# Kernel tuning notes

Measured on AMD Instinct MI355X. Metric: run time of the kernel, lower is better.

Reference implementation:

```python
import jax, jax.numpy as jnp
import numpy as np

HID = 257

def _lstm_cell(x, h, c, wih, whh, bih, bhh):
    # PyTorch gate order: i, f, g, o
    g = wih @ x + bih + whh @ h + bhh
    i, f, gg, o = jnp.split(g, 4)
    c2 = jax.nn.sigmoid(f) * c + jax.nn.sigmoid(i) * jnp.tanh(gg)
    h2 = jax.nn.sigmoid(o) * jnp.tanh(c2)
    return h2, c2

def _bilstm(x, state, p):
    # seq_len==1 bidirectional LSTM: fwd and bwd cells both see the single step
    hf, cf, hb, cb = state
    hf2, cf2 = _lstm_cell(x, hf, cf, p[0], p[1], p[2], p[3])
    hb2, cb2 = _lstm_cell(x, hb, cb, p[4], p[5], p[6], p[7])
    return jnp.concatenate([hf2, hb2]), (hf2, cf2, hb2, cb2)

def _conv_relu(x, w, b):
    y = jax.lax.conv_general_dilated(x, w, (1, 1), 'VALID', dimension_numbers=('NCHW', 'OIHW', 'NCHW'))
    return jax.nn.relu(y + b[None, :, None, None])

def _forward(src, conv1_w, conv1_b, conv2_w, conv2_b, conv3_w, conv3_b, conv4_w, conv4_b,
             conv5_w, conv5_b, conv6_w, conv6_b, fc1_w, fc1_b, fc2_w, fc2_b, fc3_w, fc3_b,
             enc_wih_f, enc_whh_f, enc_bih_f, enc_bhh_f, enc_wih_b, enc_whh_b, enc_bih_b, enc_bhh_b,
             dec_wih_f, dec_whh_f, dec_bih_f, dec_bhh_f, dec_wih_b, dec_whh_b, dec_bih_b, dec_bhh_b,
             lin_w, lin_b, maxlinelen):
    # AdaptiveMaxPool2d(32) on 128x128 == 4x4/stride-4 max pool
    x = src.reshape(1, 32, 32, 4, 32, 4).max(axis=(3, 5))
    x = _conv_relu(x, conv1_w, conv1_b)   # (1,64,30,30)
    x = _conv_relu(x, conv2_w, conv2_b)   # (1,128,28,28)
    x = _conv_relu(x, conv3_w, conv3_b)   # (1,256,26,26)
    x = _conv_relu(x, conv4_w, conv4_b)   # (1,512,24,24)
    x = _conv_relu(x, conv5_w, conv5_b)   # (1,512,22,22)
    x = _conv_relu(x, conv6_w, conv6_b)   # (1,512,21,21) (k=2)
    # AdaptiveMaxPool2d(10) on 21x21 == window-3/stride-2 max pool
    x = jax.lax.reduce_window(x, -jnp.inf, jax.lax.max, (1, 1, 3, 3), (1, 1, 2, 2), 'VALID')
    x = x.reshape(-1)                     # (51200,)
    x = jax.nn.relu(fc1_w @ x + fc1_b)
    x = jax.nn.relu(fc2_w @ x + fc2_b)
    feat = fc3_w @ x + fc3_b              # (128,)
    enc_p = (enc_wih_f, enc_whh_f, enc_bih_f, enc_bhh_f, enc_wih_b, enc_whh_b, enc_bih_b, enc_bhh_b)
    dec_p = (dec_wih_f, dec_whh_f, dec_bih_f, dec_bhh_f, dec_wih_b, dec_whh_b, dec_bih_b, dec_bhh_b)
    z = jnp.zeros((HID,), src.dtype)
    y, enc_state = _bilstm(feat, (z, z, z, z), enc_p)  # encode, zero init state
    x = lin_w @ y + lin_b
    y, state = _bilstm(x, enc_state, dec_p)            # decode seeded with encode hidden
    x = lin_w @ y + lin_b                              # out[0]
    def step(carry, _):
        xc, st = carry
        yy, st2 = _bilstm(xc, st, dec_p)
        x2 = lin_w @ yy + lin_b
        return (x2, st2), x2
    _, rest = jax.lax.scan(step, (x, state), None, length=maxlinelen - 1)
    return jnp.concatenate([x[None, :], rest], axis=0)  # (maxlinelen, 257)

def setup_inputs():
    key = jax.random.key(0)
    ks = iter(jax.random.split(key, 64))
    def W(shape, fan):
        return jax.random.normal(next(ks), shape, jnp.float32) / np.float32(np.sqrt(fan))
    d = {}
    d['src'] = jax.random.normal(next(ks), (1, 32, 128, 128), jnp.float32)
    convs = [(64, 32, 3), (128, 64, 3), (256, 128, 3), (512, 256, 3), (512, 512, 3), (512, 512, 2)]
    for i, (o, c, k) in enumerate(convs, 1):
        d['conv%d_w' % i] = W((o, c, k, k), c * k * k)
        d['conv%d_b' % i] = jnp.zeros((o,), jnp.float32)
    d['fc1_w'] = W((2048, 51200), 51200); d['fc1_b'] = jnp.zeros((2048,), jnp.float32)
    d['fc2_w'] = W((512, 2048), 2048);    d['fc2_b'] = jnp.zeros((512,), jnp.float32)
    d['fc3_w'] = W((128, 512), 512);      d['fc3_b'] = jnp.zeros((128,), jnp.float32)
    for pre, nin in (('enc', 128), ('dec', HID)):
        for dr in ('f', 'b'):
            d['%s_wih_%s' % (pre, dr)] = W((4 * HID, nin), HID)
            d['%s_whh_%s' % (pre, dr)] = W((4 * HID, HID), HID)
            d['%s_bih_%s' % (pre, dr)] = jnp.zeros((4 * HID,), jnp.float32)
            d['%s_bhh_%s' % (pre, dr)] = jnp.zeros((4 * HID,), jnp.float32)
    d['lin_w'] = W((HID, 2 * HID), 2 * HID)
    d['lin_b'] = jnp.zeros((HID,), jnp.float32)
    d['maxlinelen'] = 128
    return d

def reference(src, conv1_w, conv1_b, conv2_w, conv2_b, conv3_w, conv3_b, conv4_w, conv4_b,
              conv5_w, conv5_b, conv6_w, conv6_b, fc1_w, fc1_b, fc2_w, fc2_b, fc3_w, fc3_b,
              enc_wih_f, enc_whh_f, enc_bih_f, enc_bhh_f, enc_wih_b, enc_whh_b, enc_bih_b, enc_bhh_b,
              dec_wih_f, dec_whh_f, dec_bih_f, dec_bhh_f, dec_wih_b, dec_whh_b, dec_bih_b, dec_bhh_b,
              lin_w, lin_b, maxlinelen):
    return _forward(src, conv1_w, conv1_b, conv2_w, conv2_b, conv3_w, conv3_b, conv4_w, conv4_b,
                    conv5_w, conv5_b, conv6_w, conv6_b, fc1_w, fc1_b, fc2_w, fc2_b, fc3_w, fc3_b,
                    enc_wih_f, enc_whh_f, enc_bih_f, enc_bhh_f, enc_wih_b, enc_whh_b, enc_bih_b, enc_bhh_b,
                    dec_wih_f, dec_whh_f, dec_bih_f, dec_bhh_f, dec_wih_b, dec_whh_b, dec_bih_b, dec_bhh_b,
                    lin_w, lin_b, maxlinelen)
```

## Files before the change

kernel.cpp:

```cpp
#include <hip/hip_runtime.h>

#define DIV_UP(a,b) (((a)+(b)-1)/(b))
#define DEC_NWG 33

__device__ __forceinline__ float sigm(float x){ return 1.f/(1.f+__expf(-x)); }
__device__ __forceinline__ float tanh_f(float x){ return 1.f - 2.f/(__expf(2.f*x)+1.f); }

__device__ __forceinline__ void fma4x4(const float4 wv, const float4 xv, float acc[4][4]){
  acc[0][0] += wv.x*xv.x; acc[0][1] += wv.x*xv.y; acc[0][2] += wv.x*xv.z; acc[0][3] += wv.x*xv.w;
  acc[1][0] += wv.y*xv.x; acc[1][1] += wv.y*xv.y; acc[1][2] += wv.y*xv.z; acc[1][3] += wv.y*xv.w;
  acc[2][0] += wv.z*xv.x; acc[2][1] += wv.z*xv.y; acc[2][2] += wv.z*xv.z; acc[2][3] += wv.z*xv.w;
  acc[3][0] += wv.w*xv.x; acc[3][1] += wv.w*xv.y; acc[3][2] += wv.w*xv.z; acc[3][3] += wv.w*xv.w;
}

__global__ void k_setup(float* zreg, int n, int* cnt){
  int idx = threadIdx.x;
  if (idx == 0) *cnt = 0;
  for (int i = idx; i < n; i += 256) zreg[i] = 0.f;
}

__global__ void k_pool1(const float* __restrict__ src, float* __restrict__ out){
  int idx = blockIdx.x*256 + threadIdx.x;
  if (idx >= 32*32*32) return;
  int x = idx & 31, y = (idx>>5)&31, c = idx>>10;
  const float* p = src + ((size_t)(c*128) + y*4)*128 + x*4;
  float m = -1e30f;
  #pragma unroll
  for (int i=0;i<4;i++)
    #pragma unroll
    for (int j=0;j<4;j++) m = fmaxf(m, p[i*128+j]);
  out[idx] = m;
}

template<int KS>
__global__ __launch_bounds__(256) void k_conv_gemm(
    const float* __restrict__ in, const float* __restrict__ w,
    float* __restrict__ part,
    int Cin, int Hin, int Win, int Cout, int Hout, int Wout, int G, int kchunk)
{
  const int P = Hout*Wout;
  const int K = Cin*KS*KS;
  const int pxT = (P+63)>>6;
  int b = blockIdx.x;
  const int g = b % G; b /= G;
  const int pt = b % pxT; const int ot = b / pxT;
  const int k0 = g*kchunk;
  const int k1 = min(K, k0+kchunk);
  const int tid = threadIdx.x;
  const int tx = tid & 15, ty = tid >> 4;
  const int sp = tid & 63, sk = tid >> 6;
  int p_st = pt*64 + sp;
  bool pv = p_st < P;
  int pys = 0, pxs = 0;
  if (pv){ pys = p_st / Wout; pxs = p_st - pys*Wout; }
  __shared__ __align__(16) float Xs[16][64];
  __shared__ __align__(16) float Ws[16][68];
  float acc[4][4];
  #pragma unroll
  for (int i=0;i<4;i++)
    #pragma unroll
    for (int j=0;j<4;j++) acc[i][j]=0.f;
  for (int kb=k0; kb<k1; kb+=16){
    #pragma unroll
    for (int i=0;i<4;i++){
      int k = kb + sk + i*4;
      float v = 0.f;
      if (k < k1 && pv){
        int ic = k/(KS*KS); int t = k - ic*(KS*KS); int ky = t/KS, kx = t - ky*KS;
        v = in[((size_t)(ic*Hin) + pys+ky)*Win + (pxs+kx)];
      }
      Xs[sk+i*4][sp] = v;
    }
    #pragma unroll
    for (int i=0;i<4;i++){
      int k = kb + tx;
      int oc = ot*64 + ty + i*16;
      Ws[tx][ty+i*16] = (k < k1) ? w[(size_t)oc*K + k] : 0.f;
    }
    __syncthreads();
    #pragma unroll
    for (int kk=0;kk<16;kk++){
      float4 wv = *(const float4*)&Ws[kk][ty*4];
      float4 xv = *(const float4*)&Xs[kk][tx*4];
      fma4x4(wv, xv, acc);
    }
    __syncthreads();
  }
  float* po = part + (size_t)g*Cout*P;
  #pragma unroll
  for (int i=0;i<4;i++){
    int oc = ot*64 + ty*4 + i;
    #pragma unroll
    for (int j=0;j<4;j++){
      int p = pt*64 + tx*4 + j;
      if (p < P) po[(size_t)oc*P + p] = acc[i][j];
    }
  }
}

__global__ void k_conv_reduce(const float* __restrict__ part, const float* __restrict__ bias,
                              float* __restrict__ out, int Cout, int P, int G){
  int idx = blockIdx.x*256 + threadIdx.x;
  int total = Cout*P;
  if (idx >= total) return;
  int oc = idx / P;
  float s = bias[oc];
  for (int g=0; g<G; g++) s += part[(size_t)g*total + idx];
  out[idx] = fmaxf(s, 0.f);
}

__global__ void k_pool2(const float* __restrict__ in, float* __restrict__ out){
  int idx = blockIdx.x*256 + threadIdx.x;
  if (idx >= 51200) return;
  int x = idx % 10; int y = (idx/10)%10; int c = idx/100;
  const float* p = in + ((size_t)(c*21) + y*2)*21 + x*2;
  float m = -1e30f;
  #pragma unroll
  for (int i=0;i<3;i++)
    #pragma unroll
    for (int j=0;j<3;j++) m = fmaxf(m, p[i*21+j]);
  out[idx] = m;
}

__global__ __launch_bounds__(256) void k_fc(const float* __restrict__ w, const float* __restrict__ x,
                     const float* __restrict__ b, float* __restrict__ out, int N, int do_relu){
  int row = blockIdx.x;
  int tid = threadIdx.x;
  const float* wr = w + (size_t)row*N;
  float s = 0.f;
  for (int i = tid*4; i < N; i += 1024){
    float4 wv = *(const float4*)(wr + i);
    float4 xv = *(const float4*)(x + i);
    s += wv.x*xv.x + wv.y*xv.y + wv.z*xv.z + wv.w*xv.w;
  }
  #pragma unroll
  for (int off=32; off; off>>=1) s += __shfl_xor(s, off, 64);
  __shared__ float red[4];
  if ((tid & 63) == 0) red[tid>>6] = s;
  __syncthreads();
  if (tid == 0){
    float t = red[0]+red[1]+red[2]+red[3] + b[row];
    if (do_relu) t = fmaxf(t, 0.f);
    out[row] = t;
  }
}

__global__ __launch_bounds__(256) void k_gemm_wl(
    const float* __restrict__ wf, const float* __restrict__ wb,
    const float* __restrict__ lw, float* __restrict__ C)
{
  int b = blockIdx.x;
  int nt = b % 9; int mt = b / 9;
  int tid = threadIdx.x;
  int tx = tid&15, ty = tid>>4;
  int sp = tid&63, sk = tid>>6;
  __shared__ __align__(16) float Xs[16][64];
  __shared__ __align__(16) float Ws[16][68];
  float acc[4][4];
  #pragma unroll
  for (int i=0;i<4;i++)
    #pragma unroll
    for (int j=0;j<4;j++) acc[i][j]=0.f;
  for (int kb=0; kb<257; kb+=16){
    #pragma unroll
    for (int i=0;i<4;i++){
      int k = kb+sk+i*4;
      int col = nt*64 + sp;
      Xs[sk+i*4][sp] = (k<257 && col<514) ? lw[(size_t)k*514+col] : 0.f;
    }
    #pragma unroll
    for (int i=0;i<4;i++){
      int k = kb+tx;
      int row = mt*64 + ty + i*16;
      float v = 0.f;
      if (k<257 && row<2056)
        v = (row<1028) ? wf[(size_t)row*257+k] : wb[(size_t)(row-1028)*257+k];
      Ws[tx][ty+i*16] = v;
    }
    __syncthreads();
    #pragma unroll
    for (int kk=0;kk<16;kk++){
      float4 wv = *(const float4*)&Ws[kk][ty*4];
      float4 xv = *(const float4*)&Xs[kk][tx*4];
      fma4x4(wv, xv, acc);
    }
    __syncthreads();
  }
  #pragma unroll
  for (int i=0;i<4;i++){
    int row = mt*64 + ty*4 + i;
    #pragma unroll
    for (int j=0;j<4;j++){
      int col = nt*64 + tx*4 + j;
      if (row<2056 && col<514) C[(size_t)row*514+col] = acc[i][j];
    }
  }
}

__global__ void k_assemble(const float* __restrict__ C, const float* __restrict__ whf,
                           const float* __restrict__ whb, float* __restrict__ A){
  int idx = blockIdx.x*256+threadIdx.x;
  if (idx >= 528*4*576) return;
  int k = idx % 576;
  int g = (idx/576)&3;
  int u = idx/2304;
  float v = 0.f;
  if (u < 514 && k < 514){
    int j = (u<257)? u : u-257;
    int row = ((u<257)?0:1028) + g*257 + j;
    v = C[(size_t)row*514 + k];
    if (u<257){ if (k<257) v += whf[(size_t)(g*257+j)*257 + k]; }
    else      { if (k>=257) v += whb[(size_t)(g*257+j)*257 + (k-257)]; }
  }
  A[idx] = v;
}

__global__ void k_dvec(const float* __restrict__ wihf, const float* __restrict__ wihb,
                       const float* __restrict__ bihf, const float* __restrict__ bhhf,
                       const float* __restrict__ bihb, const float* __restrict__ bhhb,
                       const float* __restrict__ lb, float* __restrict__ dv){
  int idx = blockIdx.x*256+threadIdx.x;
  if (idx >= 528*4) return;
  int u = idx>>2, g = idx&3;
  float v = 0.f;
  if (u < 514){
    int j = (u<257)? u : u-257;
    int r = g*257+j;
    const float* wr = ((u<257)? wihf : wihb) + (size_t)r*257;
    v = (u<257) ? (bihf[r]+bhhf[r]) : (bihb[r]+bhhb[r]);
    for (int m=0;m<257;m++) v += wr[m]*lb[m];
  }
  dv[idx]=v;
}

__global__ void k_enc_gates(const float* __restrict__ wf, const float* __restrict__ wb,
                            const float* __restrict__ bihf, const float* __restrict__ bhhf,
                            const float* __restrict__ bihb, const float* __restrict__ bhhb,
                            const float* __restrict__ feat, float* __restrict__ gates){
  __shared__ float fs[128];
  int tid = threadIdx.x;
  if (tid < 128) fs[tid] = feat[tid];
  __syncthreads();
  int r = blockIdx.x*256 + tid;
  if (r >= 2056) return;
  const float* wr; float bias;
  if (r < 1028){ wr = wf + (size_t)r*128; bias = bihf[r]+bhhf[r]; }
  else { int rr = r-1028; wr = wb + (size_t)rr*128; bias = bihb[rr]+bhhb[rr]; }
  float s = bias;
  for (int m=0;m<128;m++) s += wr[m]*fs[m];
  gates[r] = s;
}

__global__ void k_enc_point(const float* __restrict__ gates, float* __restrict__ y0,
                            float* __restrict__ cinit){
  int u = blockIdx.x*256+threadIdx.x;
  if (u >= 514) return;
  int j = (u<257)? u : u-257;
  int base = (u<257)? 0 : 1028;
  float gi = gates[base + j];
  float gg = gates[base + 514 + j];
  float go = gates[base + 771 + j];
  float c = sigm(gi)*tanh_f(gg);
  float h = sigm(go)*tanh_f(c);
  y0[u] = h; cinit[u] = c;
}

__global__ __launch_bounds__(256) void k_decode(
    const float* __restrict__ A, const float* __restrict__ dv,
    const float* __restrict__ cinit, float* __restrict__ ybuf,
    float* __restrict__ Yh, int* __restrict__ cnt)
{
  const int tid = threadIdx.x;
  const int u = blockIdx.x*16 + (tid>>4);
  const int q = tid & 15;
  float w[4][36];
  {
    const float* base = A + (size_t)u*4*576 + q*36;
    #pragma unroll
    for (int g=0; g<4; g++){
      #pragma unroll
      for (int i=0;i<36;i+=4){
        float4 v = *(const float4*)(base + g*576 + i);
        w[g][i]=v.x; w[g][i+1]=v.y; w[g][i+2]=v.z; w[g][i+3]=v.w;
      }
    }
  }
  const float4 dg = *(const float4*)(dv + u*4);
  float c = cinit[u];
  __shared__ __align__(16) float ys[576];
  for (int step=0; step<128; step++){
    const float* yin = ybuf + (step&1)*576;
    float* yout = ybuf + ((step+1)&1)*576;
    for (int i=tid; i<576; i+=256)
      ys[i] = __hip_atomic_load(yin+i, __ATOMIC_RELAXED, __HIP_MEMORY_SCOPE_AGENT);
    __syncthreads();
    float s0=0.f, s1=0.f, s2=0.f, s3=0.f;
    const float4* yl4 = (const float4*)&ys[q*36];
    #pragma unroll
    for (int i=0;i<9;i++){
      float4 yv = yl4[i];
      s0 += w[0][i*4]*yv.x + w[0][i*4+1]*yv.y + w[0][i*4+2]*yv.z + w[0][i*4+3]*yv.w;
      s1 += w[1][i*4]*yv.x + w[1][i*4+1]*yv.y + w[1][i*4+2]*yv.z + w[1][i*4+3]*yv.w;
      s2 += w[2][i*4]*yv.x + w[2][i*4+1]*yv.y + w[2][i*4+2]*yv.z + w[2][i*4+3]*yv.w;
      s3 += w[3][i*4]*yv.x + w[3][i*4+1]*yv.y + w[3][i*4+2]*yv.z + w[3][i*4+3]*yv.w;
    }
    #pragma unroll
    for (int off=8; off; off>>=1){
      s0 += __shfl_xor(s0, off, 64);
      s1 += __shfl_xor(s1, off, 64);
      s2 += __shfl_xor(s2, off, 64);
      s3 += __shfl_xor(s3, off, 64);
    }
    if (q == 0){
      float ci = sigm(s1+dg.y)*c + sigm(s0+dg.x)*tanh_f(s2+dg.z);
      c = ci;
      float h = sigm(s3+dg.w)*tanh_f(ci);
      Yh[step*576 + u] = h;
      __hip_atomic_store(yout + u, h, __ATOMIC_RELAXED, __HIP_MEMORY_SCOPE_AGENT);
    }
    __syncthreads();
    if (tid == 0){
      __hip_atomic_fetch_add(cnt, 1, __ATOMIC_ACQ_REL, __HIP_MEMORY_SCOPE_AGENT);
      const int target = DEC_NWG*(step+1);
      while (__hip_atomic_load(cnt, __ATOMIC_ACQUIRE, __HIP_MEMORY_SCOPE_AGENT) < target)
        __builtin_amdgcn_s_sleep(1);
    }
    __syncthreads();
  }
}

__global__ __launch_bounds__(256) void k_final(const float* __restrict__ Yh, const float* __restrict__ lw,
                        const float* __restrict__ lb, float* __restrict__ out){
  __shared__ float ys[514];
  int t = blockIdx.x, tid = threadIdx.x;
  for (int i=tid;i<514;i+=256) ys[i] = Yh[t*576+i];
  __syncthreads();
  for (int m=tid; m<257; m+=256){
    float s = lb[m];
    const float* wr = lw + (size_t)m*514;
    for (int k=0;k<514;k++) s += wr[k]*ys[k];
    out[t*257+m] = s;
  }
}

extern "C" void kernel_launch(void* const* d_in, const int* in_sizes, int n_in,
                              void* d_out, int out_size, void* d_ws, size_t ws_size,
                              hipStream_t stream){
  const float* src  = (const float*)d_in[0];
  const float* c1w = (const float*)d_in[1];  const float* c1b = (const float*)d_in[2];
  const float* c2w = (const float*)d_in[3];  const float* c2b = (const float*)d_in[4];
  const float* c3w = (const float*)d_in[5];  const float* c3b = (const float*)d_in[6];
  const float* c4w = (const float*)d_in[7];  const float* c4b = (const float*)d_in[8];
  const float* c5w = (const float*)d_in[9];  const float* c5b = (const float*)d_in[10];
  const float* c6w = (const float*)d_in[11]; const float* c6b = (const float*)d_in[12];
  const float* fc1w= (const float*)d_in[13]; const float* fc1b= (const float*)d_in[14];
  const float* fc2w= (const float*)d_in[15]; const float* fc2b= (const float*)d_in[16];
  const float* fc3w= (const float*)d_in[17]; const float* fc3b= (const float*)d_in[18];
  const float* ewihf=(const float*)d_in[19];
  const float* ebihf=(const float*)d_in[21]; const float* ebhhf=(const float*)d_in[22];
  const float* ewihb=(const float*)d_in[23];
  const float* ebihb=(const float*)d_in[25]; const float* ebhhb=(const float*)d_in[26];
  const float* dwihf=(const float*)d_in[27]; const float* dwhhf=(const float*)d_in[28];
  const float* dbihf=(const float*)d_in[29]; const float* dbhhf=(const float*)d_in[30];
  const float* dwihb=(const float*)d_in[31]; const float* dwhhb=(const float*)d_in[32];
  const float* dbihb=(const float*)d_in[33]; const float* dbhhb=(const float*)d_in[34];
  const float* lw  = (const float*)d_in[35]; const float* lbv = (const float*)d_in[36];
  float* out = (float*)d_out;

  float* W = (float*)d_ws;
  float* cnt_f = W + 0;
  float* ybuf  = W + 64;
  float* cinit = W + 1216;
  float* gates = W + 1744;
  float* dv    = W + 3840;
  float* A     = W + 5952;
  float* C     = W + 1222464;
  float* Yh    = W + 2279296;
  float* part  = W + 2353024;
  float* X0    = W + 3532672;
  float* X1    = W + 3827584;
  float* xfc   = W + 4075392;
  float* f1    = W + 4126592;
  float* f2    = W + 4128640;
  float* feat  = W + 4129152;

  k_setup<<<1,256,0,stream>>>(ybuf, 1152+528, (int*)cnt_f);

  k_gemm_wl<<<33*9,256,0,stream>>>(dwihf, dwihb, lw, C);
  k_assemble<<<DIV_UP(528*4*576,256),256,0,stream>>>(C, dwhhf, dwhhb, A);
  k_dvec<<<DIV_UP(2112,256),256,0,stream>>>(dwihf, dwihb, dbihf, dbhhf, dbihb, dbhhb, lbv, dv);

  k_pool1<<<128,256,0,stream>>>(src, X0);
  k_conv_gemm<3><<<1*15*18,256,0,stream>>>(X0, c1w, part, 32,32,32,  64,30,30, 18, 16);
  k_conv_reduce<<<DIV_UP(64*900,256),256,0,stream>>>(part, c1b, X1, 64, 900, 18);
  k_conv_gemm<3><<<2*13*9,256,0,stream>>>(X1, c2w, part, 64,30,30, 128,28,28, 9, 64);
  k_conv_reduce<<<DIV_UP(128*784,256),256,0,stream>>>(part, c2b, X0, 128, 784, 9);
  k_conv_gemm<3><<<4*11*6,256,0,stream>>>(X0, c3w, part, 128,28,28, 256,26,26, 6, 192);
  k_conv_reduce<<<DIV_UP(256*676,256),256,0,stream>>>(part, c3b, X1, 256, 676, 6);
  k_conv_gemm<3><<<8*9*4,256,0,stream>>>(X1, c4w, part, 256,26,26, 512,24,24, 4, 576);
  k_conv_reduce<<<DIV_UP(512*576,256),256,0,stream>>>(part, c4b, X0, 512, 576, 4);
  k_conv_gemm<3><<<8*8*4,256,0,stream>>>(X0, c5w, part, 512,24,24, 512,22,22, 4, 1152);
  k_conv_reduce<<<DIV_UP(512*484,256),256,0,stream>>>(part, c5b, X1, 512, 484, 4);
  k_conv_gemm<2><<<8*7*4,256,0,stream>>>(X1, c6w, part, 512,22,22, 512,21,21, 4, 512);
  k_conv_reduce<<<DIV_UP(512*441,256),256,0,stream>>>(part, c6b, X0, 512, 441, 4);
  k_pool2<<<200,256,0,stream>>>(X0, xfc);

  k_fc<<<2048,256,0,stream>>>(fc1w, xfc, fc1b, f1, 51200, 1);
  k_fc<<<512,256,0,stream>>>(fc2w, f1, fc2b, f2, 2048, 1);
  k_fc<<<128,256,0,stream>>>(fc3w, f2, fc3b, feat, 512, 0);

  k_enc_gates<<<9,256,0,stream>>>(ewihf, ewihb, ebihf, ebhhf, ebihb, ebhhb, feat, gates);
  k_enc_point<<<3,256,0,stream>>>(gates, ybuf, cinit);

  k_decode<<<DEC_NWG,256,0,stream>>>(A, dv, cinit, ybuf, Yh, (int*)cnt_f);

  k_final<<<128,256,0,stream>>>(Yh, lw, lbv, out);
}
```

Baseline: 1.750 ms.

## Replace decoder grid barrier with poison-flagged per-step dataflow sync

The decoder previously joined all workgroups at every one of the 128 steps through a global atomic counter barrier. It now writes each step's hidden state into its own row of a history buffer that is pre-filled with a poison pattern. Readers spin on that row until no poisoned entries remain, which removes the counter and the barrier round trips and also makes the separate Yh copy unnecessary. The dvec precompute is also changed to one wavefront per row with a shuffle reduction. The poison scheme carries a risk: a real hidden value whose bits equal the poison pattern would hang the spin loop, and relaxed atomics without an acquire fence depend on per-element visibility.

```diff
diff --git a/kernel.cpp b/kernel.cpp
--- a/kernel.cpp
+++ b/kernel.cpp
@@ -2,6 +2,7 @@
 
 #define DIV_UP(a,b) (((a)+(b)-1)/(b))
 #define DEC_NWG 33
+#define POISON 0xAAAAAAAAu
 
 __device__ __forceinline__ float sigm(float x){ return 1.f/(1.f+__expf(-x)); }
 __device__ __forceinline__ float tanh_f(float x){ return 1.f - 2.f/(__expf(2.f*x)+1.f); }
@@ -13,10 +14,9 @@
   acc[3][0] += wv.w*xv.x; acc[3][1] += wv.w*xv.y; acc[3][2] += wv.w*xv.z; acc[3][3] += wv.w*xv.w;
 }
 
-__global__ void k_setup(float* zreg, int n, int* cnt){
-  int idx = threadIdx.x;
-  if (idx == 0) *cnt = 0;
-  for (int i = idx; i < n; i += 256) zreg[i] = 0.f;
+__global__ void k_setup(unsigned int* ydec){
+  int idx = blockIdx.x*256 + threadIdx.x;
+  if (idx < 128*576) ydec[576 + idx] = POISON;
 }
 
 __global__ void k_pool1(const float* __restrict__ src, float* __restrict__ out){
@@ -219,18 +219,22 @@
                        const float* __restrict__ bihf, const float* __restrict__ bhhf,
                        const float* __restrict__ bihb, const float* __restrict__ bhhb,
                        const float* __restrict__ lb, float* __restrict__ dv){
-  int idx = blockIdx.x*256+threadIdx.x;
-  if (idx >= 528*4) return;
-  int u = idx>>2, g = idx&3;
+  int row = blockIdx.x*4 + (threadIdx.x>>6);
+  if (row >= 528*4) return;
+  int u = row>>2, g = row&3;
+  int lane = threadIdx.x & 63;
+  float s = 0.f;
   float v = 0.f;
   if (u < 514){
     int j = (u<257)? u : u-257;
     int r = g*257+j;
     const float* wr = ((u<257)? wihf : wihb) + (size_t)r*257;
-    v = (u<257) ? (bihf[r]+bhhf[r]) : (bihb[r]+bhhb[r]);
-    for (int m=0;m<257;m++) v += wr[m]*lb[m];
-  }
-  dv[idx]=v;
+    for (int m=lane;m<257;m+=64) s += wr[m]*lb[m];
+    #pragma unroll
+    for (int off=32; off; off>>=1) s += __shfl_xor(s, off, 64);
+    v = s + ((u<257) ? (bihf[r]+bhhf[r]) : (bihb[r]+bhhb[r]));
+  }
+  if (lane == 0) dv[row] = v;
 }
 
 __global__ void k_enc_gates(const float* __restrict__ wf, const float* __restrict__ wb,
@@ -251,24 +255,26 @@
   gates[r] = s;
 }
 
-__global__ void k_enc_point(const float* __restrict__ gates, float* __restrict__ y0,
+__global__ void k_enc_point(const float* __restrict__ gates, float* __restrict__ ydec0,
                             float* __restrict__ cinit){
   int u = blockIdx.x*256+threadIdx.x;
-  if (u >= 514) return;
-  int j = (u<257)? u : u-257;
-  int base = (u<257)? 0 : 1028;
-  float gi = gates[base + j];
-  float gg = gates[base + 514 + j];
-  float go = gates[base + 771 + j];
-  float c = sigm(gi)*tanh_f(gg);
-  float h = sigm(go)*tanh_f(c);
-  y0[u] = h; cinit[u] = c;
-}
-
-__global__ __launch_bounds__(256) void k_decode(
+  if (u >= 528) return;
+  float h = 0.f, c = 0.f;
+  if (u < 514){
+    int j = (u<257)? u : u-257;
+    int base = (u<257)? 0 : 1028;
+    float gi = gates[base + j];
+    float gg = gates[base + 514 + j];
+    float go = gates[base + 771 + j];
+    c = sigm(gi)*tanh_f(gg);
+    h = sigm(go)*tanh_f(c);
+  }
+  ydec0[u] = h; cinit[u] = c;
+}
+
+__global__ __launch_bounds__(256,1) void k_decode(
     const float* __restrict__ A, const float* __restrict__ dv,
-    const float* __restrict__ cinit, float* __restrict__ ybuf,
-    float* __restrict__ Yh, int* __restrict__ cnt)
+    const float* __restrict__ cinit, float* __restrict__ Ydec)
 {
   const int tid = threadIdx.x;
   const int u = blockIdx.x*16 + (tid>>4);
@@ -287,15 +293,31 @@
   }
   const float4 dg = *(const float4*)(dv + u*4);
   float c = cinit[u];
-  __shared__ __align__(16) float ys[576];
+  __shared__ __align__(16) float ys[2][576];
   for (int step=0; step<128; step++){
-    const float* yin = ybuf + (step&1)*576;
-    float* yout = ybuf + ((step+1)&1)*576;
-    for (int i=tid; i<576; i+=256)
-      ys[i] = __hip_atomic_load(yin+i, __ATOMIC_RELAXED, __HIP_MEMORY_SCOPE_AGENT);
+    float* ysb = ys[step&1];
+    if (tid < 64){
+      const unsigned int* rowp = (const unsigned int*)(Ydec + (size_t)step*576);
+      unsigned int v[9];
+      while (true){
+        bool ok = true;
+        #pragma unroll
+        for (int j=0;j<9;j++){
+          int idx = tid + j*64;
+          v[j] = __hip_atomic_load(rowp + idx, __ATOMIC_RELAXED, __HIP_MEMORY_SCOPE_AGENT);
+          if (idx < 528 && v[j] == POISON) ok = false;
+        }
+        if (__all(ok)) break;
+      }
+      #pragma unroll
+      for (int j=0;j<9;j++){
+        int idx = tid + j*64;
+        ((unsigned int*)ysb)[idx] = (idx < 528) ? v[j] : 0u;
+      }
+    }
     __syncthreads();
     float s0=0.f, s1=0.f, s2=0.f, s3=0.f;
-    const float4* yl4 = (const float4*)&ys[q*36];
+    const float4* yl4 = (const float4*)&ysb[q*36];
     #pragma unroll
     for (int i=0;i<9;i++){
       float4 yv = yl4[i];
@@ -315,30 +337,22 @@
       float ci = sigm(s1+dg.y)*c + sigm(s0+dg.x)*tanh_f(s2+dg.z);
       c = ci;
       float h = sigm(s3+dg.w)*tanh_f(ci);
-      Yh[step*576 + u] = h;
-      __hip_atomic_store(yout + u, h, __ATOMIC_RELAXED, __HIP_MEMORY_SCOPE_AGENT);
-    }
-    __syncthreads();
-    if (tid == 0){
-      __hip_atomic_fetch_add(cnt, 1, __ATOMIC_ACQ_REL, __HIP_MEMORY_SCOPE_AGENT);
-      const int target = DEC_NWG*(step+1);
-      while (__hip_atomic_load(cnt, __ATOMIC_ACQUIRE, __HIP_MEMORY_SCOPE_AGENT) < target)
-        __builtin_amdgcn_s_sleep(1);
-    }
-    __syncthreads();
-  }
-}
-
-__global__ __launch_bounds__(256) void k_final(const float* __restrict__ Yh, const float* __restrict__ lw,
+      __hip_atomic_store(Ydec + (size_t)(step+1)*576 + u, h,
+                         __ATOMIC_RELAXED, __HIP_MEMORY_SCOPE_AGENT);
+    }
+  }
+}
+
+__global__ __launch_bounds__(256) void k_final(const float* __restrict__ Ydec, const float* __restrict__ lw,
                         const float* __restrict__ lb, float* __restrict__ out){
-  __shared__ float ys[514];
+  __shared__ float ysl[514];
   int t = blockIdx.x, tid = threadIdx.x;
-  for (int i=tid;i<514;i+=256) ys[i] = Yh[t*576+i];
+  for (int i=tid;i<514;i+=256) ysl[i] = Ydec[(size_t)(t+1)*576+i];
   __syncthreads();
   for (int m=tid; m<257; m+=256){
     float s = lb[m];
     const float* wr = lw + (size_t)m*514;
-    for (int k=0;k<514;k++) s += wr[k]*ys[k];
+    for (int k=0;k<514;k++) s += wr[k]*ysl[k];
     out[t*257+m] = s;
   }
 }
@@ -368,27 +382,25 @@
   float* out = (float*)d_out;
 
   float* W = (float*)d_ws;
-  float* cnt_f = W + 0;
-  float* ybuf  = W + 64;
-  float* cinit = W + 1216;
-  float* gates = W + 1744;
-  float* dv    = W + 3840;
-  float* A     = W + 5952;
-  float* C     = W + 1222464;
-  float* Yh    = W + 2279296;
-  float* part  = W + 2353024;
-  float* X0    = W + 3532672;
-  float* X1    = W + 3827584;
-  float* xfc   = W + 4075392;
-  float* f1    = W + 4126592;
-  float* f2    = W + 4128640;
-  float* feat  = W + 4129152;
-
-  k_setup<<<1,256,0,stream>>>(ybuf, 1152+528, (int*)cnt_f);
+  float* cinit = W + 0;
+  float* gates = W + 528;
+  float* dv    = W + 2584;
+  float* A     = W + 4704;
+  float* C     = W + 1221216;
+  float* Ydec  = W + 2278000;
+  float* part  = W + 2352304;
+  float* X0    = W + 3531952;
+  float* X1    = W + 3826864;
+  float* xfc   = W + 4074672;
+  float* f1    = W + 4125872;
+  float* f2    = W + 4127920;
+  float* feat  = W + 4128432;
+
+  k_setup<<<288,256,0,stream>>>((unsigned int*)Ydec);
 
   k_gemm_wl<<<33*9,256,0,stream>>>(dwihf, dwihb, lw, C);
   k_assemble<<<DIV_UP(528*4*576,256),256,0,stream>>>(C, dwhhf, dwhhb, A);
-  k_dvec<<<DIV_UP(2112,256),256,0,stream>>>(dwihf, dwihb, dbihf, dbhhf, dbihb, dbhhb, lbv, dv);
+  k_dvec<<<528,256,0,stream>>>(dwihf, dwihb, dbihf, dbhhf, dbihb, dbhhb, lbv, dv);
 
   k_pool1<<<128,256,0,stream>>>(src, X0);
   k_conv_gemm<3><<<1*15*18,256,0,stream>>>(X0, c1w, part, 32,32,32,  64,30,30, 18, 16);
@@ -410,9 +422,9 @@
   k_fc<<<128,256,0,stream>>>(fc3w, f2, fc3b, feat, 512, 0);
 
   k_enc_gates<<<9,256,0,stream>>>(ewihf, ewihb, ebihf, ebhhf, ebihb, ebhhb, feat, gates);
-  k_enc_point<<<3,256,0,stream>>>(gates, ybuf, cinit);
-
-  k_decode<<<DEC_NWG,256,0,stream>>>(A, dv, cinit, ybuf, Yh, (int*)cnt_f);
-
-  k_final<<<128,256,0,stream>>>(Yh, lw, lbv, out);
-}
+  k_enc_point<<<3,256,0,stream>>>(gates, Ydec, cinit);
+
+  k_decode<<<DEC_NWG,256,0,stream>>>(A, dv, cinit, Ydec);
+
+  k_final<<<128,256,0,stream>>>(Ydec, lw, lbv, out);
+}
```

After: 1.565 ms. 1.12x faster.
